# Kernel tuning notes

Measured on AMD Instinct MI355X. Metric: run time of the kernel, lower is better.

## Reference

```python
import jax, jax.numpy as jnp
import numpy as np

B, P, N, C = 4, 12, 1024, 64  # batch, past window, nodes, channels (in==hidden==out)


def setup_inputs() -> dict:
    key = jax.random.key(0)
    k1, k2, k3, k4, k5, k6 = jax.random.split(key, 6)
    x = jax.random.normal(k1, (B, P, N, C), dtype=jnp.float32)
    # float adjacency mask in {0,1}; force self-loops so no softmax row is empty
    A = jax.random.randint(k2, (B, P, N, N), 0, 2).astype(jnp.float32)
    A = A.at[..., jnp.arange(N), jnp.arange(N)].set(1.0)
    # learned params (nn.Linear stores weight as [out, in]; y = x @ W.T)
    W_emb = jax.random.normal(k3, (C, C), dtype=jnp.float32) / jnp.sqrt(jnp.float32(C))
    a1 = jax.random.normal(k4, (C,), dtype=jnp.float32)
    a2 = jax.random.normal(k5, (C,), dtype=jnp.float32)
    W_lin = jax.random.normal(k6, (C, C), dtype=jnp.float32) / jnp.sqrt(jnp.float32(C))
    return {"x": x, "A": A, "W_emb": W_emb, "a1": a1, "a2": a2, "W_lin": W_lin}


def reference(x, A, W_emb, a1, a2, W_lin):
    # x_emb = emb(x)  (bias-free linear)
    x_emb = jnp.einsum('bpnc,hc->bpnh', x, W_emb)            # [B,P,N,H]
    s1 = x_emb @ a1                                           # [B,P,N]
    s2 = x_emb @ a2                                           # [B,P,N]
    # additive GAT scores: a1_i + a2_j, broadcast instead of repeat
    z = jax.nn.leaky_relu(s1[..., :, None] + s2[..., None, :], 0.01)  # [B,P,N,N]
    z = jnp.where(A == 0.0, -jnp.inf, z)
    pi = jax.nn.softmax(z, axis=-1)                           # masked attention
    agg = jnp.einsum('bpij,bpjc->bpic', pi, x)                # weighted aggregation
    out = jax.nn.sigmoid(jnp.einsum('bpic,oc->bpio', agg, W_lin))
    return (out, A)
```

## Files before the change

kernel.cpp:

```cpp
#include <hip/hip_runtime.h>

typedef __attribute__((ext_vector_type(8))) __bf16 bf16x8;
typedef __attribute__((ext_vector_type(4))) float f32x4;

#define N_ 1024
#define C_ 64
#define BP_ 48

static __device__ __forceinline__ unsigned short f2bf(float f) {
    __bf16 b = (__bf16)f;
    return __builtin_bit_cast(unsigned short, b);
}
static __device__ __forceinline__ unsigned int pack2(float a, float b) {
    return (unsigned int)f2bf(a) | ((unsigned int)f2bf(b) << 16);
}

__global__ __launch_bounds__(256) void gat_pre(
    const float* __restrict__ x, const float* __restrict__ Ag,
    const float* __restrict__ Wemb,
    const float* __restrict__ a1, const float* __restrict__ a2,
    float* __restrict__ s1g, float* __restrict__ s2g,
    unsigned short* __restrict__ xP, float* __restrict__ M2part,
    unsigned short* __restrict__ Amask)
{
    __shared__ float xs[64][65];
    __shared__ float vs[2][64];
    const int t = threadIdx.x, l = t & 63, w = t >> 6;
    const int j0 = blockIdx.x * 64;
    const int bp = blockIdx.y;

    if (w == 0) {
        float v1 = 0.f, v2 = 0.f;
        #pragma unroll 8
        for (int h = 0; h < 64; ++h) {
            float we = Wemb[h * 64 + l];
            v1 = fmaf(a1[h], we, v1);
            v2 = fmaf(a2[h], we, v2);
        }
        vs[0][l] = v1; vs[1][l] = v2;
    }
    const float* xb = x + ((size_t)bp * N_ + j0) * C_;
    #pragma unroll
    for (int it = 0; it < 16; ++it)
        xs[it * 4 + w][l] = xb[(it * 4 + w) * C_ + l];
    __syncthreads();

    const int jr = t >> 2, c0 = (t & 3) * 16;
    float p1 = 0.f, p2 = 0.f;
    #pragma unroll
    for (int k = 0; k < 16; ++k) {
        float xv = xs[jr][c0 + k];
        p1 = fmaf(xv, vs[0][c0 + k], p1);
        p2 = fmaf(xv, vs[1][c0 + k], p2);
    }
    p1 += __shfl_xor(p1, 1); p1 += __shfl_xor(p1, 2);
    p2 += __shfl_xor(p2, 1); p2 += __shfl_xor(p2, 2);
    if ((l & 3) == 0) {
        s1g[bp * N_ + j0 + jr] = p1;
        s2g[bp * N_ + j0 + jr] = p2;
    }
    float m = p2;
    m = fmaxf(m, __shfl_xor(m, 4));
    m = fmaxf(m, __shfl_xor(m, 8));
    m = fmaxf(m, __shfl_xor(m, 16));
    m = fmaxf(m, __shfl_xor(m, 32));
    if (l == 0) M2part[bp * 64 + blockIdx.x * 4 + w] = m;

    const int c = t >> 2, part = t & 3;
    unsigned short* dstb = xP + (size_t)bp * C_ * N_ + (size_t)c * N_ + j0 +
                           (part >> 1) * 32 + (part & 1) * 4;
    #pragma unroll
    for (int m_ = 0; m_ < 4; ++m_) {
        unsigned int lo = pack2(xs[part * 16 + 4 * m_ + 0][c],
                                xs[part * 16 + 4 * m_ + 1][c]);
        unsigned int hi = pack2(xs[part * 16 + 4 * m_ + 2][c],
                                xs[part * 16 + 4 * m_ + 3][c]);
        *(uint2*)&dstb[m_ * 8] = make_uint2(lo, hi);
    }

    const int row0 = blockIdx.x * 64 + w * 16;
    #pragma unroll 2
    for (int rr = 0; rr < 16; ++rr) {
        const int row = row0 + rr;
        const float* Ar = Ag + ((size_t)bp * N_ + row) * N_ + 16 * l;
        unsigned int bits = 0;
        #pragma unroll
        for (int j = 0; j < 4; ++j) {
            f32x4 a = *(const f32x4*)(Ar + 4 * j);
            #pragma unroll
            for (int r = 0; r < 4; ++r)
                bits |= (a[r] != 0.f ? 1u : 0u) << (4 * j + r);
        }
        Amask[((size_t)bp * N_ + row) * 64 + l] = (unsigned short)bits;
    }
}

#define SB() __builtin_amdgcn_sched_barrier(0)

__global__ __launch_bounds__(256, 3) void gat_fused(
    const unsigned short* __restrict__ Amask, float* __restrict__ outA,
    const unsigned short* __restrict__ xP,
    const float* __restrict__ s1g, const float* __restrict__ s2g,
    const float* __restrict__ M2part,
    const float* __restrict__ Wlin, float* __restrict__ out)
{
    __shared__ unsigned short aggLDS[4][16][72];
    __shared__ float s2lds[1024];
    __shared__ float lsLDS[4][16];

    const int t = threadIdx.x, l = t & 63, w = t >> 6;
    const int i15 = l & 15, q = l >> 4;
    const int bp = blockIdx.y;
    const int ibase = blockIdx.x * 64 + w * 16;

    *(f32x4*)&s2lds[4 * t] = *(const f32x4*)&s2g[bp * N_ + 4 * t];

    float m2v = M2part[bp * 64 + l];
    #pragma unroll
    for (int off = 32; off >= 1; off >>= 1)
        m2v = fmaxf(m2v, __shfl_xor(m2v, off));
    const float M2 = m2v;
    const float s1_l = s1g[bp * N_ + ibase + i15];
    const float zr = s1_l + M2;
    const float mv = fmaxf(zr, 0.01f * zr);

    __syncthreads();

    float* oArow = outA + ((size_t)bp * N_ + ibase + i15) * N_ + q * 4;
    const unsigned short* xProw = xP + (size_t)bp * C_ * N_ + (size_t)i15 * N_ + q * 8;
    const uint2* Mrow = (const uint2*)(Amask + ((size_t)bp * N_ + ibase + i15) * 64);

    f32x4 acc[4] = {};
    float ls = 0.f;
    const int q4 = q * 4;

    bf16x8 Xa[8], Xb[8];
    uint2 Ma, Mb;

#define LOADX(Xc, kk) do {                                                    \
    _Pragma("unroll")                                                         \
    for (int nt = 0; nt < 4; ++nt)                                            \
        _Pragma("unroll")                                                     \
        for (int s = 0; s < 2; ++s)                                           \
            Xc[s * 4 + nt] = *(const bf16x8*)&xProw[(size_t)nt * 16 * N_ +    \
                                                    (kk) * 64 + s * 32];      \
    } while (0)

#define CONSUME(Xc, Mc, kk) do {                                              \
    const int jrel = (kk) * 64;                                               \
                                          \
    f32x4 Ev[4];                                                              \
    _Pragma("unroll")                                                         \
    for (int g = 0; g < 4; ++g) {                                             \
        const f32x4 s2v = *(const f32x4*)&s2lds[jrel + g * 16 + q4];          \
        _Pragma("unroll")                                                     \
        for (int r = 0; r < 4; ++r) {                                         \
            float zz = s1_l + s2v[r];                                         \
            zz = fmaxf(zz, 0.01f * zz);                                       \
            Ev[g][r] = __expf(zz - mv);                                       \
        }                                                                     \
    }                                                                         \
    SB();                                                                     \
                        \
    f32x4 P[4];                                                               \
    _Pragma("unroll")                                                         \
    for (int g = 0; g < 4; ++g) {                                             \
        const unsigned int wbits = (g < 2) ? Mc.x : Mc.y;                     \
        const int sh = (g & 1) * 16 + q4;                                     \
        f32x4 oAv;                                                            \
        _Pragma("unroll")                                                     \
        for (int r = 0; r < 4; ++r) {                                         \
            float bf = (float)((wbits >> (sh + r)) & 1u);                     \
            oAv[r] = bf;                                                      \
            P[g][r] = bf * Ev[g][r];                                          \
            ls += P[g][r];                                                    \
        }                                                                     \
        *(f32x4*)(oArow + jrel + g * 16) = oAv;                               \
    }                                                                         \
    uint4 u0 = make_uint4(pack2(P[0][0], P[0][1]), pack2(P[0][2], P[0][3]),   \
                          pack2(P[1][0], P[1][1]), pack2(P[1][2], P[1][3]));  \
    uint4 u1 = make_uint4(pack2(P[2][0], P[2][1]), pack2(P[2][2], P[2][3]),   \
                          pack2(P[3][0], P[3][1]), pack2(P[3][2], P[3][3]));  \
    bf16x8 af0 = __builtin_bit_cast(bf16x8, u0);                              \
    bf16x8 af1 = __builtin_bit_cast(bf16x8, u1);                              \
    _Pragma("unroll")                                                         \
    for (int nt = 0; nt < 4; ++nt)                                            \
        acc[nt] = __builtin_amdgcn_mfma_f32_16x16x32_bf16(af0, Xc[nt],        \
                                                          acc[nt], 0, 0, 0);  \
    _Pragma("unroll")                                                         \
    for (int nt = 0; nt < 4; ++nt)                                            \
        acc[nt] = __builtin_amdgcn_mfma_f32_16x16x32_bf16(af1, Xc[4 + nt],    \
                                                          acc[nt], 0, 0, 0);  \
    } while (0)

    LOADX(Xa, 0); Ma = Mrow[0];
    #pragma unroll 1
    for (int k = 0; k < 16; k += 2) {
        SB();
        Mb = Mrow[k + 1]; LOADX(Xb, k + 1);
        SB();
        CONSUME(Xa, Ma, k);
        SB();
        if (k + 2 < 16) { Ma = Mrow[k + 2]; LOADX(Xa, k + 2); }
        SB();
        CONSUME(Xb, Mb, k + 1);
    }
    SB();
#undef LOADX
#undef CONSUME

    ls += __shfl_xor(ls, 16);
    ls += __shfl_xor(ls, 32);
    if (q == 0) lsLDS[w][i15] = ls;
    const f32x4 lsq = *(const f32x4*)&lsLDS[w][4 * q];

    unsigned short* aggl = &aggLDS[w][0][0];
    #pragma unroll
    for (int nt = 0; nt < 4; ++nt)
        #pragma unroll
        for (int r = 0; r < 4; ++r)
            aggl[(q * 4 + r) * 72 + nt * 16 + i15] = f2bf(acc[nt][r] / lsq[r]);

    f32x4 d2[4] = {};
    #pragma unroll
    for (int s = 0; s < 2; ++s) {
        bf16x8 af = *(const bf16x8*)&aggl[i15 * 72 + s * 32 + q * 8];
        #pragma unroll
        for (int nt = 0; nt < 4; ++nt) {
            const float* wp = Wlin + (size_t)(nt * 16 + i15) * C_ + s * 32 + q * 8;
            f32x4 w0 = *(const f32x4*)wp;
            f32x4 w1 = *(const f32x4*)(wp + 4);
            bf16x8 bfr;
            #pragma unroll
            for (int jj = 0; jj < 4; ++jj) { bfr[jj] = (__bf16)w0[jj]; bfr[4 + jj] = (__bf16)w1[jj]; }
            d2[nt] = __builtin_amdgcn_mfma_f32_16x16x32_bf16(af, bfr, d2[nt], 0, 0, 0);
        }
    }
    float* orow = out + ((size_t)bp * N_ + ibase) * C_;
    #pragma unroll
    for (int nt = 0; nt < 4; ++nt)
        #pragma unroll
        for (int r = 0; r < 4; ++r)
            orow[(size_t)(q * 4 + r) * C_ + nt * 16 + i15] =
                1.f / (1.f + __expf(-d2[nt][r]));
}

extern "C" void kernel_launch(void* const* d_in, const int* in_sizes, int n_in,
                              void* d_out, int out_size, void* d_ws, size_t ws_size,
                              hipStream_t stream) {
    const float* x    = (const float*)d_in[0];
    const float* Ag   = (const float*)d_in[1];
    const float* Wemb = (const float*)d_in[2];
    const float* a1   = (const float*)d_in[3];
    const float* a2   = (const float*)d_in[4];
    const float* Wlin = (const float*)d_in[5];
    float* out  = (float*)d_out;
    float* outA = out + (size_t)BP_ * N_ * C_;

    float* s1g = (float*)d_ws;
    float* s2g = s1g + BP_ * N_;
    float* M2part = s2g + BP_ * N_;
    unsigned short* xP = (unsigned short*)(M2part + BP_ * 64);
    unsigned short* Amask = xP + (size_t)BP_ * C_ * N_;

    gat_pre<<<dim3(16, BP_), dim3(256), 0, stream>>>(x, Ag, Wemb, a1, a2,
                                                     s1g, s2g, xP, M2part, Amask);
    gat_fused<<<dim3(16, BP_), dim3(256), 0, stream>>>(Amask, outA, xP, s1g, s2g,
                                                       M2part, Wlin, out);
}
```

Baseline: 430.5 us.

## Move adjacency copy and bitmask packing into a dedicated streaming kernel

A new grid-stride kernel reads A once with nontemporal loads. In the same pass it writes the A output copy with nontemporal stores and packs the bitmask. The preprocessing kernel no longer reads A, and the fused attention kernel no longer rebuilds and stores the A output from the mask bits. The aim is a simple, bandwidth-friendly pass over the 200MB of A traffic, with the attention kernel relieved of its heavy output stores. In exchange it adds a third kernel launch and serialises the streaming pass before the compute kernels.

After: 650.2 us. +51.0%, slower.

```diff
diff --git a/kernel.cpp b/kernel.cpp
--- a/kernel.cpp
+++ b/kernel.cpp
@@ -15,13 +15,35 @@
     return (unsigned int)f2bf(a) | ((unsigned int)f2bf(b) << 16);
 }
 
+__global__ __launch_bounds__(256) void gat_pack(
+    const float* __restrict__ Ag, float* __restrict__ outA,
+    unsigned short* __restrict__ Amask)
+{
+    const size_t seg0 = (size_t)blockIdx.x * 256 + threadIdx.x;
+    const size_t stride = (size_t)2048 * 256;
+    #pragma unroll 2
+    for (int it = 0; it < 6; ++it) {
+        const size_t seg = seg0 + (size_t)it * stride;
+        const f32x4* src = (const f32x4*)(Ag + seg * 16);
+        f32x4* dst = (f32x4*)(outA + seg * 16);
+        unsigned int bits = 0;
+        #pragma unroll
+        for (int j = 0; j < 4; ++j) {
+            f32x4 a = __builtin_nontemporal_load(src + j);
+            __builtin_nontemporal_store(a, dst + j);
+            #pragma unroll
+            for (int r = 0; r < 4; ++r)
+                bits |= (a[r] != 0.f ? 1u : 0u) << (4 * j + r);
+        }
+        Amask[seg] = (unsigned short)bits;
+    }
+}
+
 __global__ __launch_bounds__(256) void gat_pre(
-    const float* __restrict__ x, const float* __restrict__ Ag,
-    const float* __restrict__ Wemb,
+    const float* __restrict__ x, const float* __restrict__ Wemb,
     const float* __restrict__ a1, const float* __restrict__ a2,
     float* __restrict__ s1g, float* __restrict__ s2g,
-    unsigned short* __restrict__ xP, float* __restrict__ M2part,
-    unsigned short* __restrict__ Amask)
+    unsigned short* __restrict__ xP, float* __restrict__ M2part)
 {
     __shared__ float xs[64][65];
     __shared__ float vs[2][64];
@@ -77,28 +99,12 @@
                                 xs[part * 16 + 4 * m_ + 3][c]);
         *(uint2*)&dstb[m_ * 8] = make_uint2(lo, hi);
     }
-
-    const int row0 = blockIdx.x * 64 + w * 16;
-    #pragma unroll 2
-    for (int rr = 0; rr < 16; ++rr) {
-        const int row = row0 + rr;
-        const float* Ar = Ag + ((size_t)bp * N_ + row) * N_ + 16 * l;
-        unsigned int bits = 0;
-        #pragma unroll
-        for (int j = 0; j < 4; ++j) {
-            f32x4 a = *(const f32x4*)(Ar + 4 * j);
-            #pragma unroll
-            for (int r = 0; r < 4; ++r)
-                bits |= (a[r] != 0.f ? 1u : 0u) << (4 * j + r);
-        }
-        Amask[((size_t)bp * N_ + row) * 64 + l] = (unsigned short)bits;
-    }
 }
 
 #define SB() __builtin_amdgcn_sched_barrier(0)
 
 __global__ __launch_bounds__(256, 3) void gat_fused(
-    const unsigned short* __restrict__ Amask, float* __restrict__ outA,
+    const unsigned short* __restrict__ Amask,
     const unsigned short* __restrict__ xP,
     const float* __restrict__ s1g, const float* __restrict__ s2g,
     const float* __restrict__ M2part,
@@ -126,7 +132,6 @@
 
     __syncthreads();
 
-    float* oArow = outA + ((size_t)bp * N_ + ibase + i15) * N_ + q * 4;
     const unsigned short* xProw = xP + (size_t)bp * C_ * N_ + (size_t)i15 * N_ + q * 8;
     const uint2* Mrow = (const uint2*)(Amask + ((size_t)bp * N_ + ibase + i15) * 64);
 
@@ -148,7 +153,6 @@
 
 #define CONSUME(Xc, Mc, kk) do {                                              \
     const int jrel = (kk) * 64;                                               \
-                                          \
     f32x4 Ev[4];                                                              \
     _Pragma("unroll")                                                         \
     for (int g = 0; g < 4; ++g) {                                             \
@@ -161,21 +165,17 @@
         }                                                                     \
     }                                                                         \
     SB();                                                                     \
-                        \
     f32x4 P[4];                                                               \
     _Pragma("unroll")                                                         \
     for (int g = 0; g < 4; ++g) {                                             \
         const unsigned int wbits = (g < 2) ? Mc.x : Mc.y;                     \
         const int sh = (g & 1) * 16 + q4;                                     \
-        f32x4 oAv;                                                            \
         _Pragma("unroll")                                                     \
         for (int r = 0; r < 4; ++r) {                                         \
             float bf = (float)((wbits >> (sh + r)) & 1u);                     \
-            oAv[r] = bf;                                                      \
             P[g][r] = bf * Ev[g][r];                                          \
             ls += P[g][r];                                                    \
         }                                                                     \
-        *(f32x4*)(oArow + jrel + g * 16) = oAv;                               \
     }                                                                         \
     uint4 u0 = make_uint4(pack2(P[0][0], P[0][1]), pack2(P[0][2], P[0][3]),   \
                           pack2(P[1][0], P[1][1]), pack2(P[1][2], P[1][3]));  \
@@ -263,8 +263,9 @@
     unsigned short* xP = (unsigned short*)(M2part + BP_ * 64);
     unsigned short* Amask = xP + (size_t)BP_ * C_ * N_;
 
-    gat_pre<<<dim3(16, BP_), dim3(256), 0, stream>>>(x, Ag, Wemb, a1, a2,
-                                                     s1g, s2g, xP, M2part, Amask);
-    gat_fused<<<dim3(16, BP_), dim3(256), 0, stream>>>(Amask, outA, xP, s1g, s2g,
+    gat_pack<<<dim3(2048), dim3(256), 0, stream>>>(Ag, outA, Amask);
+    gat_pre<<<dim3(16, BP_), dim3(256), 0, stream>>>(x, Wemb, a1, a2,
+                                                     s1g, s2g, xP, M2part);
+    gat_fused<<<dim3(16, BP_), dim3(256), 0, stream>>>(Amask, xP, s1g, s2g,
                                                        M2part, Wlin, out);
 }
```
